# Performance work log

Measured on AMD Instinct MI355X. Metric: run time of the kernel, lower is better.

## Reference

```python
import jax, jax.numpy as jnp
import numpy as np

ALPHA = 50.0
EPS = 1e-12  # torch F.normalize eps


def setup_inputs() -> dict:
    key = jax.random.key(0)
    k1, k2 = jax.random.split(key)
    N, C, H, W_sp, K = 64, 128, 64, 64, 64
    x = jax.random.normal(k1, (N, C, H, W_sp), dtype=jnp.float32)
    # centroids.permute(1,0): shape [C, K]; orthogonal-ish init approximated by scaled gaussian
    W = jax.random.normal(k2, (C, K), dtype=jnp.float32) * (1.0 / np.sqrt(C))
    bias = jnp.zeros((K,), dtype=jnp.float32)
    return {"x": x, "W": W, "bias": bias}


def _l2norm(v, axis):
    return v / jnp.maximum(jnp.linalg.norm(v, axis=axis, keepdims=True), EPS)


def reference(x, W, bias):
    N, C, H, W_sp = x.shape
    K = W.shape[1]
    x = _l2norm(x, axis=1)                      # normalize over channels
    xf = x.reshape(N, C, H * W_sp)              # [N, C, P]
    Wn = _l2norm(W, axis=0)                     # column-normalized weight [C, K]
    # soft assignment logits, computed directly in [N, K, P] layout
    sa_logits = jnp.einsum('ncp,ck->nkp', xf, Wn)
    sa = jax.nn.softmax((sa_logits + bias[None, :, None]) * ALPHA, axis=1)  # over clusters
    # VLAD via two GEMM-like contractions instead of the [N,K,C,P] residual tensor:
    # vlad[n,k,c] = sum_p sa[n,k,p] * xf[n,c,p] - W[c,k] * sum_p sa[n,k,p]
    vlad = jnp.einsum('nkp,ncp->nkc', sa, xf) - sa.sum(axis=-1)[:, :, None] * W.T[None]
    vlad = _l2norm(vlad, axis=2)                # intra-normalize per cluster
    vlad = vlad.reshape(N, K * C)
    vlad = _l2norm(vlad, axis=1)                # global L2
    return (vlad, sa_logits)                    # original returns soft_assign_ permuted to [N, K, P]
```

## Files before the change

### kernel.cpp

```cpp
#include <hip/hip_runtime.h>
#include <math.h>

#define ALPHA 50.0f
#define EPS 1e-12f

constexpr int N = 64, C = 128, P = 4096, K = 64;
constexpr int NCH2 = 8;

typedef short short8_t __attribute__((ext_vector_type(8)));
typedef short short4_t __attribute__((ext_vector_type(4)));
typedef float f4 __attribute__((ext_vector_type(4)));
typedef unsigned int u32x4 __attribute__((ext_vector_type(4)));
typedef unsigned int u32x2 __attribute__((ext_vector_type(2)));

__device__ __forceinline__ unsigned short f2bf(float f) {
    union { float f; unsigned u; } v; v.f = f;
    unsigned r = (v.u + 0x7FFFu + ((v.u >> 16) & 1u)) >> 16;
    return (unsigned short)r;
}

__device__ __forceinline__ unsigned cvtpk(float lo, float hi) {
    unsigned r;
    asm("v_cvt_pk_bf16_f32 %0, %1, %2" : "=v"(r) : "v"(lo), "v"(hi));
    return r;
}

__device__ __forceinline__ void bar_lds() {
    asm volatile("s_waitcnt lgkmcnt(0)" ::: "memory");
    __builtin_amdgcn_s_barrier();
}

__global__ __launch_bounds__(256, 2) void k_fused(
    const float* __restrict__ x, const float* __restrict__ W,
    const float* __restrict__ bias, float* __restrict__ logits,
    float* __restrict__ vlad_part, float* __restrict__ Spart,
    float* __restrict__ ss2acc)
{
    __shared__ __align__(16) char smem[69632];
    unsigned short* xsT  = (unsigned short*)smem;
    unsigned short* xsN  = (unsigned short*)(smem + 17408);
    float*          saf  = (float*)(smem + 36864);
    unsigned short* sa2s = (unsigned short*)(smem + 54272);
    float*          denom= (float*)(smem + 63488);
    float*          invs = (float*)(smem + 67840);
    float*          rfin = (float*)(smem + 68096);
    float*          red  = (float*)(smem + 68352);
    float*          biass= (float*)(smem + 69376);
    float*          Wl   = (float*)smem;
    unsigned short* wnl  = (unsigned short*)(smem + 36864);

    const int tid  = threadIdx.x;
    const int n    = blockIdx.x >> 3;
    const int blk8 = blockIdx.x & 7;
    const int pbase = blk8 * 512;

    const int w = tid >> 6, lane = tid & 63;
    const int q = lane >> 4, l15 = lane & 15;
    const int pxg = tid & 15, cg = tid >> 4;

    if (blockIdx.x == 0 && tid < 64) ss2acc[tid] = 0.f;
    if (tid < K) biass[tid] = bias[tid] * ALPHA;

    const float* xrow = x + (size_t)n * C * P + pbase + 4 * pxg;
    float4 va[8], vb[8];
    short8_t af[4];

    {
        float4 wv[8];
        #pragma unroll
        for (int it = 0; it < 8; ++it)
            wv[it] = *(const float4*)&W[(size_t)(tid + it * 256) * 4];
        #pragma unroll
        for (int j = 0; j < 8; ++j)
            va[j] = *(const float4*)&xrow[(size_t)(8 * cg + j) * P];
        #pragma unroll
        for (int it = 0; it < 8; ++it) {
            const int idx4 = tid + it * 256;
            *(float4*)&Wl[(idx4 >> 4) * 68 + (idx4 & 15) * 4] = wv[it];
        }
        bar_lds();
        {
            const int k = tid & 63, part = tid >> 6;
            float s = 0.f;
            #pragma unroll
            for (int i = 0; i < 32; ++i) {
                float v = Wl[(part * 32 + i) * 68 + k];
                s = fmaf(v, v, s);
            }
            red[tid] = s;
        }
        bar_lds();
        if (tid < 64)
            invs[tid] = 1.0f / fmaxf(
                sqrtf(red[tid] + red[64 + tid] + red[128 + tid] + red[192 + tid]), EPS);
        bar_lds();
        #pragma unroll
        for (int it = 0; it < 32; ++it) {
            const int idx = tid + it * 256;
            const int k = idx >> 7, c = idx & 127;
            wnl[k * 128 + c] = f2bf(Wl[c * 68 + k] * invs[k]);
        }
        bar_lds();
        #pragma unroll
        for (int c0 = 0; c0 < 4; ++c0)
            af[c0] = *(const short8_t*)&wnl[(16 * w + l15) * 128 + c0 * 32 + 8 * q];
    }

    f4 acc2[8];
    #pragma unroll
    for (int ct = 0; ct < 8; ++ct) acc2[ct] = (f4){0.f, 0.f, 0.f, 0.f};
    float Sreg = 0.f;

    const int pbT8 = 8 * (cg ^ (pxg & 7));
    const int l4 = l15 >> 2;

    for (int ch = 0; ch < 8; ++ch) {
        if (ch < 7) {
            const float* xb = xrow + (ch + 1) * 64;
            #pragma unroll
            for (int j = 0; j < 8; ++j)
                vb[j] = *(const float4*)&xb[(size_t)(8 * cg + j) * P];
        }
        bar_lds();
        const int p0 = pbase + ch * 64;
        const float* vf = (const float*)va;

        float pss[4] = {0.f, 0.f, 0.f, 0.f};
        #pragma unroll
        for (int j = 0; j < 8; ++j)
            #pragma unroll
            for (int i = 0; i < 4; ++i)
                pss[i] = fmaf(vf[j * 4 + i], vf[j * 4 + i], pss[i]);
        float* rd2 = saf;
        #pragma unroll
        for (int i = 0; i < 4; ++i) rd2[(4 * pxg + i) * 17 + cg] = pss[i];

        #pragma unroll
        for (int i = 0; i < 4; ++i) {
            u32x4 t;
            #pragma unroll
            for (int jj = 0; jj < 4; ++jj)
                t[jj] = cvtpk(vf[(2 * jj) * 4 + i], vf[(2 * jj + 1) * 4 + i]);
            *(u32x4*)&xsT[(4 * pxg + i) * 136 + pbT8] = t;
        }
        #pragma unroll
        for (int j = 0; j < 8; ++j) {
            u32x2 t2;
            t2[0] = cvtpk(vf[j * 4 + 0], vf[j * 4 + 1]);
            t2[1] = cvtpk(vf[j * 4 + 2], vf[j * 4 + 3]);
            *(u32x2*)&xsN[(8 * cg + j) * 76 + 4 * pxg] = t2;
        }
        bar_lds();

        if (tid < 64) {
            float s = 0.f;
            #pragma unroll
            for (int g = 0; g < 16; ++g) s += rd2[tid * 17 + g];
            invs[tid] = 1.0f / fmaxf(sqrtf(s), EPS);
        }
        f4 acc1[4];
        #pragma unroll
        for (int t = 0; t < 4; ++t) acc1[t] = (f4){0.f, 0.f, 0.f, 0.f};
        __builtin_amdgcn_s_setprio(1);
        #pragma unroll
        for (int c0 = 0; c0 < 4; ++c0)
            #pragma unroll
            for (int pxt = 0; pxt < 4; ++pxt) {
                const int pb = (4 * c0 + q) ^ (4 * (pxt & 1) + l4);
                short8_t bf = *(const short8_t*)&xsT[(pxt * 16 + l15) * 136 + pb * 8];
                acc1[pxt] = __builtin_amdgcn_mfma_f32_16x16x32_bf16(af[c0], bf, acc1[pxt], 0, 0, 0);
            }
        __builtin_amdgcn_s_setprio(0);
        bar_lds();

        float* lgp = logits + (size_t)n * K * P + p0;
        float bz[4];
        #pragma unroll
        for (int r = 0; r < 4; ++r) bz[r] = biass[16 * w + 4 * q + r];
        #pragma unroll
        for (int pxt = 0; pxt < 4; ++pxt) {
            const int pxl = pxt * 16 + l15;
            const float iv = invs[pxl];
            float psum = 0.f;
            #pragma unroll
            for (int r = 0; r < 4; ++r) {
                const int k = 16 * w + 4 * q + r;
                const float lv = acc1[pxt][r] * iv;
                __builtin_nontemporal_store(lv, &lgp[(size_t)k * P + pxl]);
                const float e = __expf(fmaf(lv, ALPHA, bz[r]));
                saf[k * 68 + pxl] = e;
                psum += e;
            }
            denom[(4 * w + q) * 68 + pxl] = psum;
        }
        bar_lds();
        if (tid < 64) {
            float d = 0.f;
            #pragma unroll
            for (int g = 0; g < 16; ++g) d += denom[g * 68 + tid];
            rfin[tid] = 1.0f / d;
        }
        bar_lds();

        {
            const float* sp = &saf[lane * 68 + 16 * w];
            const float* rp = &rfin[16 * w];
            const float* ip = &invs[16 * w];
            float s = 0.f;
            unsigned pk[8];
            #pragma unroll
            for (int m = 0; m < 4; ++m) {
                f4 e  = *(const f4*)&sp[4 * m];
                f4 rf = *(const f4*)&rp[4 * m];
                f4 iv = *(const f4*)&ip[4 * m];
                s += e[0] * rf[0]; s += e[1] * rf[1];
                s += e[2] * rf[2]; s += e[3] * rf[3];
                const float v0 = e[0] * (rf[0] * iv[0]);
                const float v1 = e[1] * (rf[1] * iv[1]);
                const float v2 = e[2] * (rf[2] * iv[2]);
                const float v3 = e[3] * (rf[3] * iv[3]);
                pk[2 * m]     = cvtpk(v0, v1);
                pk[2 * m + 1] = cvtpk(v2, v3);
            }
            Sreg += s;
            *(u32x4*)&sa2s[lane * 72 + 16 * w]     = (u32x4){pk[0], pk[1], pk[2], pk[3]};
            *(u32x4*)&sa2s[lane * 72 + 16 * w + 8] = (u32x4){pk[4], pk[5], pk[6], pk[7]};
        }
        bar_lds();

        short8_t a2[2];
        #pragma unroll
        for (int kit = 0; kit < 2; ++kit)
            a2[kit] = *(const short8_t*)&sa2s[(16 * w + l15) * 72 + kit * 32 + 8 * q];
        __builtin_amdgcn_s_setprio(1);
        #pragma unroll
        for (int ct = 0; ct < 8; ++ct)
            #pragma unroll
            for (int kit = 0; kit < 2; ++kit) {
                const unsigned short* bp = &xsN[(ct * 16 + l15) * 76 + kit * 32 + 8 * q];
                short4_t b0 = *(const short4_t*)bp;
                short4_t b1 = *(const short4_t*)(bp + 4);
                short8_t bb;
                bb[0] = b0[0]; bb[1] = b0[1]; bb[2] = b0[2]; bb[3] = b0[3];
                bb[4] = b1[0]; bb[5] = b1[1]; bb[6] = b1[2]; bb[7] = b1[3];
                acc2[ct] = __builtin_amdgcn_mfma_f32_16x16x32_bf16(a2[kit], bb, acc2[ct], 0, 0, 0);
            }
        __builtin_amdgcn_s_setprio(0);

        if (ch < 7) {
            #pragma unroll
            for (int j = 0; j < 8; ++j) va[j] = vb[j];
        }
    }

    float* vp = vlad_part + ((size_t)blk8 * N + n) * (size_t)(K * C);
    #pragma unroll
    for (int ct = 0; ct < 8; ++ct)
        #pragma unroll
        for (int r = 0; r < 4; ++r)
            vp[(16 * w + 4 * q + r) * C + ct * 16 + l15] = acc2[ct][r];

    red[tid] = Sreg;
    __syncthreads();
    if (tid < 64)
        Spart[((size_t)blk8 * N + n) * K + tid] =
            red[tid] + red[64 + tid] + red[128 + tid] + red[192 + tid];
}

__global__ __launch_bounds__(256) void k_post1(
    const float* __restrict__ vlad_part, const float* __restrict__ W,
    const float* __restrict__ Spart, float* __restrict__ out,
    float* __restrict__ ss2acc)
{
    __shared__ float red[16];
    const int tid = threadIdx.x;
    const int n  = blockIdx.x >> 2;
    const int kq = blockIdx.x & 3;
    const int kl = tid >> 4;
    const int ci = tid & 15;
    const int k  = kq * 16 + kl;
    const int c0 = ci * 8;

    float Sk = 0.f;
    #pragma unroll
    for (int ch = 0; ch < NCH2; ++ch) Sk += Spart[(size_t)(ch * N + n) * K + k];

    float v[8];
    #pragma unroll
    for (int l = 0; l < 8; ++l) v[l] = 0.f;
    #pragma unroll
    for (int ch = 0; ch < NCH2; ++ch) {
        const float* vp = vlad_part + ((size_t)(ch * N + n) * K + k) * C + c0;
        float4 a = *(const float4*)&vp[0];
        float4 b = *(const float4*)&vp[4];
        v[0] += a.x; v[1] += a.y; v[2] += a.z; v[3] += a.w;
        v[4] += b.x; v[5] += b.y; v[6] += b.z; v[7] += b.w;
    }

    float ss = 0.f;
    #pragma unroll
    for (int l = 0; l < 8; ++l) {
        float val = v[l] - W[(size_t)(c0 + l) * K + k] * Sk;
        v[l] = val;
        ss = fmaf(val, val, ss);
    }
    ss += __shfl_xor(ss, 1);
    ss += __shfl_xor(ss, 2);
    ss += __shfl_xor(ss, 4);
    ss += __shfl_xor(ss, 8);
    const float inv1 = 1.0f / fmaxf(sqrtf(ss), EPS);
    float ss2 = 0.f;
    #pragma unroll
    for (int l = 0; l < 8; ++l) { v[l] *= inv1; ss2 = fmaf(v[l], v[l], ss2); }
    ss2 += __shfl_xor(ss2, 1);
    ss2 += __shfl_xor(ss2, 2);
    ss2 += __shfl_xor(ss2, 4);
    ss2 += __shfl_xor(ss2, 8);
    if (ci == 0) red[kl] = ss2;
    __syncthreads();
    if (tid == 0) {
        float t = 0.f;
        #pragma unroll
        for (int i = 0; i < 16; ++i) t += red[i];
        atomicAdd(&ss2acc[n], t);
    }

    float* op = out + (size_t)n * K * C + (size_t)k * C + c0;
    *(float4*)&op[0] = (float4){v[0], v[1], v[2], v[3]};
    *(float4*)&op[4] = (float4){v[4], v[5], v[6], v[7]};
}

__global__ __launch_bounds__(256) void k_post2(
    float* __restrict__ out, const float* __restrict__ ss2acc)
{
    const int n   = blockIdx.x >> 2;
    const int seg = blockIdx.x & 3;
    const float inv2 = 1.0f / fmaxf(sqrtf(ss2acc[n]), EPS);
    float* p = out + (size_t)n * K * C + (size_t)seg * 2048 + (size_t)threadIdx.x * 8;
    float4 a = *(const float4*)&p[0];
    float4 b = *(const float4*)&p[4];
    a.x *= inv2; a.y *= inv2; a.z *= inv2; a.w *= inv2;
    b.x *= inv2; b.y *= inv2; b.z *= inv2; b.w *= inv2;
    *(float4*)&p[0] = a;
    *(float4*)&p[4] = b;
}

extern "C" void kernel_launch(void* const* d_in, const int* in_sizes, int n_in,
                              void* d_out, int out_size, void* d_ws, size_t ws_size,
                              hipStream_t stream)
{
    const float* x    = (const float*)d_in[0];
    const float* W    = (const float*)d_in[1];
    const float* bias = (const float*)d_in[2];

    float* out_vlad   = (float*)d_out;
    float* out_logits = (float*)d_out + (size_t)N * K * C;

    float* ss2acc     = (float*)((char*)d_ws + 16384);
    float* Spart      = (float*)((char*)d_ws + 32768);
    float* vlad_part  = (float*)((char*)d_ws + 32768 + 131072);

    k_fused<<<dim3(N * NCH2), dim3(256), 0, stream>>>(
        x, W, bias, out_logits, vlad_part, Spart, ss2acc);
    k_post1<<<dim3(N * 4), dim3(256), 0, stream>>>(vlad_part, W, Spart, out_vlad, ss2acc);
    k_post2<<<dim3(N * 4), dim3(256), 0, stream>>>(out_vlad, ss2acc);
}
```

Before: 237.6 us.

## Split pixels over 16 blocks per image, shrink LDS for 3 blocks/CU

Doubles the pixel-dimension split so each block handles 256 pixels, which doubles the grid to 1024 blocks. The shared-memory layout is compacted (saf aliased over the staging area, no separate wnl/rfin buffers) so that three blocks fit per CU. One barrier per chunk is removed by computing softmax denominators per wave and broadcasting them with shuffles, and the normalized-weight MFMA fragments are built directly from registers. The cost is twice as many partial VLAD tiles written to the workspace and reduced later, plus a longer prologue relative to each block's work.

After: 276.2 us. +16.2%, slower.

```diff
diff --git a/kernel.cpp b/kernel.cpp
--- a/kernel.cpp
+++ b/kernel.cpp
@@ -5,7 +5,7 @@
 #define EPS 1e-12f
 
 constexpr int N = 64, C = 128, P = 4096, K = 64;
-constexpr int NCH2 = 8;
+constexpr int NCH2 = 16;
 
 typedef short short8_t __attribute__((ext_vector_type(8)));
 typedef short short4_t __attribute__((ext_vector_type(4)));
@@ -30,29 +30,27 @@
     __builtin_amdgcn_s_barrier();
 }
 
-__global__ __launch_bounds__(256, 2) void k_fused(
+__global__ __launch_bounds__(256, 3) void k_fused(
     const float* __restrict__ x, const float* __restrict__ W,
     const float* __restrict__ bias, float* __restrict__ logits,
     float* __restrict__ vlad_part, float* __restrict__ Spart,
     float* __restrict__ ss2acc)
 {
-    __shared__ __align__(16) char smem[69632];
+    __shared__ __align__(16) char smem[51968];
     unsigned short* xsT  = (unsigned short*)smem;
     unsigned short* xsN  = (unsigned short*)(smem + 17408);
-    float*          saf  = (float*)(smem + 36864);
-    unsigned short* sa2s = (unsigned short*)(smem + 54272);
-    float*          denom= (float*)(smem + 63488);
-    float*          invs = (float*)(smem + 67840);
-    float*          rfin = (float*)(smem + 68096);
-    float*          red  = (float*)(smem + 68352);
-    float*          biass= (float*)(smem + 69376);
+    float*          saf  = (float*)smem;
+    unsigned short* sa2s = (unsigned short*)(smem + 36864);
+    float*          denom= (float*)(smem + 46080);
+    float*          invs = (float*)(smem + 50432);
+    float*          biass= (float*)(smem + 50688);
+    float*          red  = (float*)(smem + 50944);
     float*          Wl   = (float*)smem;
-    unsigned short* wnl  = (unsigned short*)(smem + 36864);
 
     const int tid  = threadIdx.x;
-    const int n    = blockIdx.x >> 3;
-    const int blk8 = blockIdx.x & 7;
-    const int pbase = blk8 * 512;
+    const int n    = blockIdx.x >> 4;
+    const int blk16= blockIdx.x & 15;
+    const int pbase = blk16 * 256;
 
     const int w = tid >> 6, lane = tid & 63;
     const int q = lane >> 4, l15 = lane & 15;
@@ -94,16 +92,15 @@
             invs[tid] = 1.0f / fmaxf(
                 sqrtf(red[tid] + red[64 + tid] + red[128 + tid] + red[192 + tid]), EPS);
         bar_lds();
-        #pragma unroll
-        for (int it = 0; it < 32; ++it) {
-            const int idx = tid + it * 256;
-            const int k = idx >> 7, c = idx & 127;
-            wnl[k * 128 + c] = f2bf(Wl[c * 68 + k] * invs[k]);
-        }
-        bar_lds();
-        #pragma unroll
-        for (int c0 = 0; c0 < 4; ++c0)
-            af[c0] = *(const short8_t*)&wnl[(16 * w + l15) * 128 + c0 * 32 + 8 * q];
+        {
+            const float cv = invs[16 * w + l15];
+            #pragma unroll
+            for (int c0 = 0; c0 < 4; ++c0)
+                #pragma unroll
+                for (int j = 0; j < 8; ++j)
+                    af[c0][j] = (short)f2bf(
+                        Wl[(c0 * 32 + 8 * q + j) * 68 + 16 * w + l15] * cv);
+        }
     }
 
     f4 acc2[8];
@@ -114,8 +111,8 @@
     const int pbT8 = 8 * (cg ^ (pxg & 7));
     const int l4 = l15 >> 2;
 
-    for (int ch = 0; ch < 8; ++ch) {
-        if (ch < 7) {
+    for (int ch = 0; ch < 4; ++ch) {
+        if (ch < 3) {
             const float* xb = xrow + (ch + 1) * 64;
             #pragma unroll
             for (int j = 0; j < 8; ++j)
@@ -131,7 +128,7 @@
             #pragma unroll
             for (int i = 0; i < 4; ++i)
                 pss[i] = fmaf(vf[j * 4 + i], vf[j * 4 + i], pss[i]);
-        float* rd2 = saf;
+        float* rd2 = denom;
         #pragma unroll
         for (int i = 0; i < 4; ++i) rd2[(4 * pxg + i) * 17 + cg] = pss[i];
 
@@ -194,31 +191,34 @@
             denom[(4 * w + q) * 68 + pxl] = psum;
         }
         bar_lds();
-        if (tid < 64) {
-            float d = 0.f;
-            #pragma unroll
-            for (int g = 0; g < 16; ++g) d += denom[g * 68 + tid];
-            rfin[tid] = 1.0f / d;
-        }
-        bar_lds();
 
         {
+            float dinv = 0.f;
+            if (lane < 16) {
+                const int pxr = 16 * w + lane;
+                float dd = 0.f;
+                #pragma unroll
+                for (int g = 0; g < 16; ++g) dd += denom[g * 68 + pxr];
+                dinv = 1.0f / dd;
+            }
             const float* sp = &saf[lane * 68 + 16 * w];
-            const float* rp = &rfin[16 * w];
             const float* ip = &invs[16 * w];
             float s = 0.f;
             unsigned pk[8];
             #pragma unroll
             for (int m = 0; m < 4; ++m) {
                 f4 e  = *(const f4*)&sp[4 * m];
-                f4 rf = *(const f4*)&rp[4 * m];
                 f4 iv = *(const f4*)&ip[4 * m];
-                s += e[0] * rf[0]; s += e[1] * rf[1];
-                s += e[2] * rf[2]; s += e[3] * rf[3];
-                const float v0 = e[0] * (rf[0] * iv[0]);
-                const float v1 = e[1] * (rf[1] * iv[1]);
-                const float v2 = e[2] * (rf[2] * iv[2]);
-                const float v3 = e[3] * (rf[3] * iv[3]);
+                const float r0 = __shfl(dinv, 4 * m + 0);
+                const float r1 = __shfl(dinv, 4 * m + 1);
+                const float r2 = __shfl(dinv, 4 * m + 2);
+                const float r3 = __shfl(dinv, 4 * m + 3);
+                s += e[0] * r0; s += e[1] * r1;
+                s += e[2] * r2; s += e[3] * r3;
+                const float v0 = e[0] * (r0 * iv[0]);
+                const float v1 = e[1] * (r1 * iv[1]);
+                const float v2 = e[2] * (r2 * iv[2]);
+                const float v3 = e[3] * (r3 * iv[3]);
                 pk[2 * m]     = cvtpk(v0, v1);
                 pk[2 * m + 1] = cvtpk(v2, v3);
             }
@@ -247,13 +247,13 @@
             }
         __builtin_amdgcn_s_setprio(0);
 
-        if (ch < 7) {
+        if (ch < 3) {
             #pragma unroll
             for (int j = 0; j < 8; ++j) va[j] = vb[j];
         }
     }
 
-    float* vp = vlad_part + ((size_t)blk8 * N + n) * (size_t)(K * C);
+    float* vp = vlad_part + ((size_t)blk16 * N + n) * (size_t)(K * C);
     #pragma unroll
     for (int ct = 0; ct < 8; ++ct)
         #pragma unroll
@@ -263,7 +263,7 @@
     red[tid] = Sreg;
     __syncthreads();
     if (tid < 64)
-        Spart[((size_t)blk8 * N + n) * K + tid] =
+        Spart[((size_t)blk16 * N + n) * K + tid] =
             red[tid] + red[64 + tid] + red[128 + tid] + red[192 + tid];
 }
 
@@ -358,7 +358,7 @@
 
     float* ss2acc     = (float*)((char*)d_ws + 16384);
     float* Spart      = (float*)((char*)d_ws + 32768);
-    float* vlad_part  = (float*)((char*)d_ws + 32768 + 131072);
+    float* vlad_part  = (float*)((char*)d_ws + 32768 + 262144);
 
     k_fused<<<dim3(N * NCH2), dim3(256), 0, stream>>>(
         x, W, bias, out_logits, vlad_part, Spart, ss2acc);
```

## Give each wave its own pixel slice so softmax needs no block-wide LDS reductions

Applied to the files above, without the earlier changes.

The fused kernel now has each wave own 16 pixels across all 64 clusters. The per-pixel channel norm and softmax denominator are computed with wave shuffles instead of LDS round trips and several block barriers. The normalized centroid fragments and biases for all four cluster tiles are held in registers, which shrinks LDS and drops the fp32 exp staging buffer. The cost is more register pressure (16 A fragments, 16 exp values, 16 S partials), and the double-buffered x prefetch is replaced by an in-place reload. k_post1 is also rebalanced to use twice as many blocks with 4 channels per thread.

New measurement: 236.1 us (median of 2 runs). Within noise of the previous version (-0.6%).

```diff
diff --git a/kernel.cpp b/kernel.cpp
--- a/kernel.cpp
+++ b/kernel.cpp
@@ -36,18 +36,15 @@
     float* __restrict__ vlad_part, float* __restrict__ Spart,
     float* __restrict__ ss2acc)
 {
-    __shared__ __align__(16) char smem[69632];
+    __shared__ __align__(16) char smem[47616];
     unsigned short* xsT  = (unsigned short*)smem;
     unsigned short* xsN  = (unsigned short*)(smem + 17408);
-    float*          saf  = (float*)(smem + 36864);
-    unsigned short* sa2s = (unsigned short*)(smem + 54272);
-    float*          denom= (float*)(smem + 63488);
-    float*          invs = (float*)(smem + 67840);
-    float*          rfin = (float*)(smem + 68096);
-    float*          red  = (float*)(smem + 68352);
-    float*          biass= (float*)(smem + 69376);
+    unsigned short* sa2s = (unsigned short*)(smem + 36864);
+    float*          biass= (float*)(smem + 46080);
+    float*          Sb2  = (float*)(smem + 46336);
+    float*          red  = Sb2;
+    float*          cinv = (float*)(smem + 47360);
     float*          Wl   = (float*)smem;
-    unsigned short* wnl  = (unsigned short*)(smem + 36864);
 
     const int tid  = threadIdx.x;
     const int n    = blockIdx.x >> 3;
@@ -56,14 +53,15 @@
 
     const int w = tid >> 6, lane = tid & 63;
     const int q = lane >> 4, l15 = lane & 15;
-    const int pxg = tid & 15, cg = tid >> 4;
+    const int c2 = lane >> 2, px4 = lane & 3;
 
     if (blockIdx.x == 0 && tid < 64) ss2acc[tid] = 0.f;
     if (tid < K) biass[tid] = bias[tid] * ALPHA;
 
-    const float* xrow = x + (size_t)n * C * P + pbase + 4 * pxg;
-    float4 va[8], vb[8];
-    short8_t af[4];
+    const float* xw = x + (size_t)n * C * P + pbase + 16 * w + 4 * px4 + (size_t)(8 * c2) * P;
+    float4 va[8];
+    short8_t af[4][4];
+    float bzv[16];
 
     {
         float4 wv[8];
@@ -71,8 +69,7 @@
         for (int it = 0; it < 8; ++it)
             wv[it] = *(const float4*)&W[(size_t)(tid + it * 256) * 4];
         #pragma unroll
-        for (int j = 0; j < 8; ++j)
-            va[j] = *(const float4*)&xrow[(size_t)(8 * cg + j) * P];
+        for (int j = 0; j < 8; ++j) va[j] = *(const float4*)&xw[(size_t)j * P];
         #pragma unroll
         for (int it = 0; it < 8; ++it) {
             const int idx4 = tid + it * 256;
@@ -91,38 +88,34 @@
         }
         bar_lds();
         if (tid < 64)
-            invs[tid] = 1.0f / fmaxf(
+            cinv[tid] = 1.0f / fmaxf(
                 sqrtf(red[tid] + red[64 + tid] + red[128 + tid] + red[192 + tid]), EPS);
         bar_lds();
         #pragma unroll
-        for (int it = 0; it < 32; ++it) {
-            const int idx = tid + it * 256;
-            const int k = idx >> 7, c = idx & 127;
-            wnl[k * 128 + c] = f2bf(Wl[c * 68 + k] * invs[k]);
-        }
-        bar_lds();
-        #pragma unroll
-        for (int c0 = 0; c0 < 4; ++c0)
-            af[c0] = *(const short8_t*)&wnl[(16 * w + l15) * 128 + c0 * 32 + 8 * q];
+        for (int kt = 0; kt < 4; ++kt) {
+            const float cv = cinv[16 * kt + l15];
+            #pragma unroll
+            for (int s = 0; s < 4; ++s)
+                #pragma unroll
+                for (int j = 0; j < 8; ++j)
+                    af[kt][s][j] = (short)f2bf(
+                        Wl[(s * 32 + 8 * q + j) * 68 + 16 * kt + l15] * cv);
+            #pragma unroll
+            for (int r = 0; r < 4; ++r) bzv[4 * kt + r] = biass[16 * kt + 4 * q + r];
+        }
+        bar_lds();
     }
 
     f4 acc2[8];
     #pragma unroll
     for (int ct = 0; ct < 8; ++ct) acc2[ct] = (f4){0.f, 0.f, 0.f, 0.f};
-    float Sreg = 0.f;
-
-    const int pbT8 = 8 * (cg ^ (pxg & 7));
-    const int l4 = l15 >> 2;
+    float Sreg[16];
+    #pragma unroll
+    for (int i = 0; i < 16; ++i) Sreg[i] = 0.f;
+
+    unsigned short* xsTw = xsT + w * 2176;
 
     for (int ch = 0; ch < 8; ++ch) {
-        if (ch < 7) {
-            const float* xb = xrow + (ch + 1) * 64;
-            #pragma unroll
-            for (int j = 0; j < 8; ++j)
-                vb[j] = *(const float4*)&xb[(size_t)(8 * cg + j) * P];
-        }
-        bar_lds();
-        const int p0 = pbase + ch * 64;
         const float* vf = (const float*)va;
 
         float pss[4] = {0.f, 0.f, 0.f, 0.f};
@@ -131,9 +124,16 @@
             #pragma unroll
             for (int i = 0; i < 4; ++i)
                 pss[i] = fmaf(vf[j * 4 + i], vf[j * 4 + i], pss[i]);
-        float* rd2 = saf;
-        #pragma unroll
-        for (int i = 0; i < 4; ++i) rd2[(4 * pxg + i) * 17 + cg] = pss[i];
+        #pragma unroll
+        for (int i = 0; i < 4; ++i) {
+            pss[i] += __shfl_xor(pss[i], 4);
+            pss[i] += __shfl_xor(pss[i], 8);
+            pss[i] += __shfl_xor(pss[i], 16);
+            pss[i] += __shfl_xor(pss[i], 32);
+        }
+        float iv4[4];
+        #pragma unroll
+        for (int i = 0; i < 4; ++i) iv4[i] = 1.0f / fmaxf(sqrtf(pss[i]), EPS);
 
         #pragma unroll
         for (int i = 0; i < 4; ++i) {
@@ -141,116 +141,92 @@
             #pragma unroll
             for (int jj = 0; jj < 4; ++jj)
                 t[jj] = cvtpk(vf[(2 * jj) * 4 + i], vf[(2 * jj + 1) * 4 + i]);
-            *(u32x4*)&xsT[(4 * pxg + i) * 136 + pbT8] = t;
+            const int row = 4 * px4 + i;
+            *(u32x4*)&xsTw[row * 136 + 8 * (c2 ^ (row & 7))] = t;
         }
         #pragma unroll
         for (int j = 0; j < 8; ++j) {
             u32x2 t2;
             t2[0] = cvtpk(vf[j * 4 + 0], vf[j * 4 + 1]);
             t2[1] = cvtpk(vf[j * 4 + 2], vf[j * 4 + 3]);
-            *(u32x2*)&xsN[(8 * cg + j) * 76 + 4 * pxg] = t2;
-        }
-        bar_lds();
-
-        if (tid < 64) {
-            float s = 0.f;
-            #pragma unroll
-            for (int g = 0; g < 16; ++g) s += rd2[tid * 17 + g];
-            invs[tid] = 1.0f / fmaxf(sqrtf(s), EPS);
-        }
+            *(u32x2*)&xsN[(8 * c2 + j) * 76 + 16 * w + 4 * px4] = t2;
+        }
+        if (ch < 7) {
+            #pragma unroll
+            for (int j = 0; j < 8; ++j)
+                va[j] = *(const float4*)&xw[(size_t)j * P + (ch + 1) * 64];
+        }
+        asm volatile("s_waitcnt lgkmcnt(0)" ::: "memory");
+        __builtin_amdgcn_sched_barrier(0);
+
         f4 acc1[4];
         #pragma unroll
         for (int t = 0; t < 4; ++t) acc1[t] = (f4){0.f, 0.f, 0.f, 0.f};
         __builtin_amdgcn_s_setprio(1);
         #pragma unroll
-        for (int c0 = 0; c0 < 4; ++c0)
-            #pragma unroll
-            for (int pxt = 0; pxt < 4; ++pxt) {
-                const int pb = (4 * c0 + q) ^ (4 * (pxt & 1) + l4);
-                short8_t bf = *(const short8_t*)&xsT[(pxt * 16 + l15) * 136 + pb * 8];
-                acc1[pxt] = __builtin_amdgcn_mfma_f32_16x16x32_bf16(af[c0], bf, acc1[pxt], 0, 0, 0);
+        for (int s = 0; s < 4; ++s) {
+            short8_t bf = *(const short8_t*)&xsTw[l15 * 136 + 8 * ((4 * s + q) ^ (l15 & 7))];
+            #pragma unroll
+            for (int kt = 0; kt < 4; ++kt)
+                acc1[kt] = __builtin_amdgcn_mfma_f32_16x16x32_bf16(af[kt][s], bf, acc1[kt], 0, 0, 0);
+        }
+        __builtin_amdgcn_s_setprio(0);
+
+        const float s0 = __shfl(iv4[0], l15 >> 2);
+        const float s1 = __shfl(iv4[1], l15 >> 2);
+        const float s2 = __shfl(iv4[2], l15 >> 2);
+        const float s3 = __shfl(iv4[3], l15 >> 2);
+        const int li = l15 & 3;
+        const float myiv = (li == 0) ? s0 : (li == 1) ? s1 : (li == 2) ? s2 : s3;
+
+        float* lgp = logits + (size_t)n * K * P + pbase + ch * 64 + 16 * w + l15;
+        float ev[16];
+        float dl = 0.f;
+        #pragma unroll
+        for (int kt = 0; kt < 4; ++kt)
+            #pragma unroll
+            for (int r = 0; r < 4; ++r) {
+                const float lv = acc1[kt][r] * myiv;
+                __builtin_nontemporal_store(lv, &lgp[(size_t)(16 * kt + 4 * q + r) * P]);
+                const float e = __expf(fmaf(lv, ALPHA, bzv[4 * kt + r]));
+                ev[4 * kt + r] = e;
+                dl += e;
             }
-        __builtin_amdgcn_s_setprio(0);
-        bar_lds();
-
-        float* lgp = logits + (size_t)n * K * P + p0;
-        float bz[4];
-        #pragma unroll
-        for (int r = 0; r < 4; ++r) bz[r] = biass[16 * w + 4 * q + r];
-        #pragma unroll
-        for (int pxt = 0; pxt < 4; ++pxt) {
-            const int pxl = pxt * 16 + l15;
-            const float iv = invs[pxl];
-            float psum = 0.f;
+        dl += __shfl_xor(dl, 16);
+        dl += __shfl_xor(dl, 32);
+        const float rf = 1.0f / dl;
+        const float sc = rf * myiv;
+        #pragma unroll
+        for (int kt = 0; kt < 4; ++kt)
             #pragma unroll
             for (int r = 0; r < 4; ++r) {
-                const int k = 16 * w + 4 * q + r;
-                const float lv = acc1[pxt][r] * iv;
-                __builtin_nontemporal_store(lv, &lgp[(size_t)k * P + pxl]);
-                const float e = __expf(fmaf(lv, ALPHA, bz[r]));
-                saf[k * 68 + pxl] = e;
-                psum += e;
+                const float e = ev[4 * kt + r];
+                Sreg[4 * kt + r] += e * rf;
+                sa2s[(16 * kt + 4 * q + r) * 72 + 16 * w + l15] = f2bf(e * sc);
             }
-            denom[(4 * w + q) * 68 + pxl] = psum;
-        }
-        bar_lds();
-        if (tid < 64) {
-            float d = 0.f;
-            #pragma unroll
-            for (int g = 0; g < 16; ++g) d += denom[g * 68 + tid];
-            rfin[tid] = 1.0f / d;
-        }
         bar_lds();
 
         {
-            const float* sp = &saf[lane * 68 + 16 * w];
-            const float* rp = &rfin[16 * w];
-            const float* ip = &invs[16 * w];
-            float s = 0.f;
-            unsigned pk[8];
-            #pragma unroll
-            for (int m = 0; m < 4; ++m) {
-                f4 e  = *(const f4*)&sp[4 * m];
-                f4 rf = *(const f4*)&rp[4 * m];
-                f4 iv = *(const f4*)&ip[4 * m];
-                s += e[0] * rf[0]; s += e[1] * rf[1];
-                s += e[2] * rf[2]; s += e[3] * rf[3];
-                const float v0 = e[0] * (rf[0] * iv[0]);
-                const float v1 = e[1] * (rf[1] * iv[1]);
-                const float v2 = e[2] * (rf[2] * iv[2]);
-                const float v3 = e[3] * (rf[3] * iv[3]);
-                pk[2 * m]     = cvtpk(v0, v1);
-                pk[2 * m + 1] = cvtpk(v2, v3);
-            }
-            Sreg += s;
-            *(u32x4*)&sa2s[lane * 72 + 16 * w]     = (u32x4){pk[0], pk[1], pk[2], pk[3]};
-            *(u32x4*)&sa2s[lane * 72 + 16 * w + 8] = (u32x4){pk[4], pk[5], pk[6], pk[7]};
-        }
-        bar_lds();
-
-        short8_t a2[2];
-        #pragma unroll
-        for (int kit = 0; kit < 2; ++kit)
-            a2[kit] = *(const short8_t*)&sa2s[(16 * w + l15) * 72 + kit * 32 + 8 * q];
-        __builtin_amdgcn_s_setprio(1);
-        #pragma unroll
-        for (int ct = 0; ct < 8; ++ct)
-            #pragma unroll
-            for (int kit = 0; kit < 2; ++kit) {
-                const unsigned short* bp = &xsN[(ct * 16 + l15) * 76 + kit * 32 + 8 * q];
-                short4_t b0 = *(const short4_t*)bp;
-                short4_t b1 = *(const short4_t*)(bp + 4);
-                short8_t bb;
-                bb[0] = b0[0]; bb[1] = b0[1]; bb[2] = b0[2]; bb[3] = b0[3];
-                bb[4] = b1[0]; bb[5] = b1[1]; bb[6] = b1[2]; bb[7] = b1[3];
-                acc2[ct] = __builtin_amdgcn_mfma_f32_16x16x32_bf16(a2[kit], bb, acc2[ct], 0, 0, 0);
-            }
-        __builtin_amdgcn_s_setprio(0);
-
-        if (ch < 7) {
-            #pragma unroll
-            for (int j = 0; j < 8; ++j) va[j] = vb[j];
-        }
+            short8_t a2[2];
+            #pragma unroll
+            for (int kit = 0; kit < 2; ++kit)
+                a2[kit] = *(const short8_t*)&sa2s[(16 * w + l15) * 72 + kit * 32 + 8 * q];
+            __builtin_amdgcn_s_setprio(1);
+            #pragma unroll
+            for (int ct = 0; ct < 8; ++ct)
+                #pragma unroll
+                for (int kit = 0; kit < 2; ++kit) {
+                    const unsigned short* bp = &xsN[(ct * 16 + l15) * 76 + kit * 32 + 8 * q];
+                    short4_t b0 = *(const short4_t*)bp;
+                    short4_t b1 = *(const short4_t*)(bp + 4);
+                    short8_t bb;
+                    bb[0] = b0[0]; bb[1] = b0[1]; bb[2] = b0[2]; bb[3] = b0[3];
+                    bb[4] = b1[0]; bb[5] = b1[1]; bb[6] = b1[2]; bb[7] = b1[3];
+                    acc2[ct] = __builtin_amdgcn_mfma_f32_16x16x32_bf16(a2[kit], bb, acc2[ct], 0, 0, 0);
+                }
+            __builtin_amdgcn_s_setprio(0);
+        }
+        bar_lds();
     }
 
     float* vp = vlad_part + ((size_t)blk8 * N + n) * (size_t)(K * C);
@@ -260,11 +236,22 @@
         for (int r = 0; r < 4; ++r)
             vp[(16 * w + 4 * q + r) * C + ct * 16 + l15] = acc2[ct][r];
 
-    red[tid] = Sreg;
+    #pragma unroll
+    for (int i = 0; i < 16; ++i) {
+        Sreg[i] += __shfl_xor(Sreg[i], 1);
+        Sreg[i] += __shfl_xor(Sreg[i], 2);
+        Sreg[i] += __shfl_xor(Sreg[i], 4);
+        Sreg[i] += __shfl_xor(Sreg[i], 8);
+    }
+    if (l15 == 0) {
+        #pragma unroll
+        for (int i = 0; i < 16; ++i)
+            Sb2[w * 64 + 16 * (i >> 2) + 4 * q + (i & 3)] = Sreg[i];
+    }
     __syncthreads();
     if (tid < 64)
         Spart[((size_t)blk8 * N + n) * K + tid] =
-            red[tid] + red[64 + tid] + red[128 + tid] + red[192 + tid];
+            Sb2[tid] + Sb2[64 + tid] + Sb2[128 + tid] + Sb2[192 + tid];
 }
 
 __global__ __launch_bounds__(256) void k_post1(
@@ -272,34 +259,32 @@
     const float* __restrict__ Spart, float* __restrict__ out,
     float* __restrict__ ss2acc)
 {
-    __shared__ float red[16];
+    __shared__ float red[8];
     const int tid = threadIdx.x;
-    const int n  = blockIdx.x >> 2;
-    const int kq = blockIdx.x & 3;
-    const int kl = tid >> 4;
-    const int ci = tid & 15;
-    const int k  = kq * 16 + kl;
-    const int c0 = ci * 8;
+    const int n  = blockIdx.x >> 3;
+    const int kq = blockIdx.x & 7;
+    const int kl = tid >> 5;
+    const int ci = tid & 31;
+    const int k  = kq * 8 + kl;
+    const int c0 = ci * 4;
 
     float Sk = 0.f;
     #pragma unroll
     for (int ch = 0; ch < NCH2; ++ch) Sk += Spart[(size_t)(ch * N + n) * K + k];
 
-    float v[8];
-    #pragma unroll
-    for (int l = 0; l < 8; ++l) v[l] = 0.f;
+    float v[4];
+    #pragma unroll
+    for (int l = 0; l < 4; ++l) v[l] = 0.f;
     #pragma unroll
     for (int ch = 0; ch < NCH2; ++ch) {
         const float* vp = vlad_part + ((size_t)(ch * N + n) * K + k) * C + c0;
         float4 a = *(const float4*)&vp[0];
-        float4 b = *(const float4*)&vp[4];
         v[0] += a.x; v[1] += a.y; v[2] += a.z; v[3] += a.w;
-        v[4] += b.x; v[5] += b.y; v[6] += b.z; v[7] += b.w;
     }
 
     float ss = 0.f;
     #pragma unroll
-    for (int l = 0; l < 8; ++l) {
+    for (int l = 0; l < 4; ++l) {
         float val = v[l] - W[(size_t)(c0 + l) * K + k] * Sk;
         v[l] = val;
         ss = fmaf(val, val, ss);
@@ -308,26 +293,27 @@
     ss += __shfl_xor(ss, 2);
     ss += __shfl_xor(ss, 4);
     ss += __shfl_xor(ss, 8);
+    ss += __shfl_xor(ss, 16);
     const float inv1 = 1.0f / fmaxf(sqrtf(ss), EPS);
     float ss2 = 0.f;
     #pragma unroll
-    for (int l = 0; l < 8; ++l) { v[l] *= inv1; ss2 = fmaf(v[l], v[l], ss2); }
+    for (int l = 0; l < 4; ++l) { v[l] *= inv1; ss2 = fmaf(v[l], v[l], ss2); }
     ss2 += __shfl_xor(ss2, 1);
     ss2 += __shfl_xor(ss2, 2);
     ss2 += __shfl_xor(ss2, 4);
     ss2 += __shfl_xor(ss2, 8);
+    ss2 += __shfl_xor(ss2, 16);
     if (ci == 0) red[kl] = ss2;
     __syncthreads();
     if (tid == 0) {
         float t = 0.f;
         #pragma unroll
-        for (int i = 0; i < 16; ++i) t += red[i];
+        for (int i = 0; i < 8; ++i) t += red[i];
         atomicAdd(&ss2acc[n], t);
     }
 
     float* op = out + (size_t)n * K * C + (size_t)k * C + c0;
     *(float4*)&op[0] = (float4){v[0], v[1], v[2], v[3]};
-    *(float4*)&op[4] = (float4){v[4], v[5], v[6], v[7]};
 }
 
 __global__ __launch_bounds__(256) void k_post2(
@@ -362,6 +348,6 @@
 
     k_fused<<<dim3(N * NCH2), dim3(256), 0, stream>>>(
         x, W, bias, out_logits, vlad_part, Spart, ss2acc);
-    k_post1<<<dim3(N * 4), dim3(256), 0, stream>>>(vlad_part, W, Spart, out_vlad, ss2acc);
+    k_post1<<<dim3(N * 8), dim3(256), 0, stream>>>(vlad_part, W, Spart, out_vlad, ss2acc);
     k_post2<<<dim3(N * 4), dim3(256), 0, stream>>>(out_vlad, ss2acc);
 }
```
